# Kernel optimization log

Hardware: AMD Instinct MI355X
Metric: run time of the kernel (lower is better)

## Reference

```python
import jax, jax.numpy as jnp
import numpy as np

ORDER = 2  # diffusion steps per support
NUM_LAYERS = 2


def gconv(z, supports, W, b):
    # z: [B,N,C]; supports: [S,N,N]; concat [z, S1 z, S1^2 z, S2 z, S2^2 z] -> dense proj
    feats = [z]
    for si in range(supports.shape[0]):
        s = supports[si]
        zk = z
        for _ in range(ORDER):
            zk = jnp.einsum('mn,bnc->bmc', s, zk)
            feats.append(zk)
    zcat = jnp.concatenate(feats, axis=-1)  # [B,N,C*(1+S*ORDER)]
    return zcat @ W + b


def dcgru_cell(x, h, supports, Wg, bg, Wc, bc):
    H = h.shape[-1]
    zr = jax.nn.sigmoid(gconv(jnp.concatenate([x, h], axis=-1), supports, Wg, bg))
    z, r = zr[..., :H], zr[..., H:]
    hc = jnp.tanh(gconv(jnp.concatenate([x, r * h], axis=-1), supports, Wc, bc))
    return z * h + (1.0 - z) * hc


def setup_inputs() -> dict:
    key = jax.random.key(0)
    ks = jax.random.split(key, 32)
    B, T, N, D_IN, H = 64, 12, 325, 2, 128
    K = 1 + 2 * ORDER  # 5 diffusion matrices
    inp = {}
    inp['source'] = jax.random.normal(ks[0], (B, T, N, D_IN), jnp.float32)
    inp['targets'] = jax.random.normal(ks[1], (B, T, N, D_IN), jnp.float32)
    u = jax.random.uniform(ks[2], (2, N, N), jnp.float32)
    inp['supports'] = u / jnp.sum(u, axis=-1, keepdims=True)  # row-stochastic random walks
    sc = 0.05
    inp['enc_Wg0'] = sc * jax.random.normal(ks[3], ((D_IN + H) * K, 2 * H), jnp.float32)
    inp['enc_bg0'] = jnp.zeros((2 * H,), jnp.float32)
    inp['enc_Wc0'] = sc * jax.random.normal(ks[4], ((D_IN + H) * K, H), jnp.float32)
    inp['enc_bc0'] = jnp.zeros((H,), jnp.float32)
    inp['enc_Wg1'] = sc * jax.random.normal(ks[5], ((H + H) * K, 2 * H), jnp.float32)
    inp['enc_bg1'] = jnp.zeros((2 * H,), jnp.float32)
    inp['enc_Wc1'] = sc * jax.random.normal(ks[6], ((H + H) * K, H), jnp.float32)
    inp['enc_bc1'] = jnp.zeros((H,), jnp.float32)
    inp['dec_Wg0'] = sc * jax.random.normal(ks[7], ((D_IN + H) * K, 2 * H), jnp.float32)
    inp['dec_bg0'] = jnp.zeros((2 * H,), jnp.float32)
    inp['dec_Wc0'] = sc * jax.random.normal(ks[8], ((D_IN + H) * K, H), jnp.float32)
    inp['dec_bc0'] = jnp.zeros((H,), jnp.float32)
    inp['dec_Wg1'] = sc * jax.random.normal(ks[9], ((H + H) * K, 2 * H), jnp.float32)
    inp['dec_bg1'] = jnp.zeros((2 * H,), jnp.float32)
    inp['dec_Wc1'] = sc * jax.random.normal(ks[10], ((H + H) * K, H), jnp.float32)
    inp['dec_bc1'] = jnp.zeros((H,), jnp.float32)
    inp['Wp'] = sc * jax.random.normal(ks[11], (H, D_IN), jnp.float32)
    inp['bp'] = jnp.zeros((D_IN,), jnp.float32)
    return inp


def _forward(source, targets, supports,
             enc_Wg0, enc_bg0, enc_Wc0, enc_bc0, enc_Wg1, enc_bg1, enc_Wc1, enc_bc1,
             dec_Wg0, dec_bg0, dec_Wc0, dec_bc0, dec_Wg1, dec_bg1, dec_Wc1, dec_bc1,
             Wp, bp):
    B, T_in, N, D_in = source.shape
    T_out = targets.shape[1]
    enc_params = [(enc_Wg0, enc_bg0, enc_Wc0, enc_bc0), (enc_Wg1, enc_bg1, enc_Wc1, enc_bc1)]
    dec_params = [(dec_Wg0, dec_bg0, dec_Wc0, dec_bc0), (dec_Wg1, dec_bg1, dec_Wc1, dec_bc1)]

    # ---- encoder: per layer, scan over time ----
    cur = jnp.swapaxes(source, 0, 1)  # [T,B,N,C]
    enc_finals = []
    for (Wg, bg, Wc, bc) in enc_params:
        H = Wc.shape[-1]
        h0 = jnp.zeros((B, N, H), source.dtype)
        def step(h, xt, Wg=Wg, bg=bg, Wc=Wc, bc=bc):
            h2 = dcgru_cell(xt, h, supports, Wg, bg, Wc, bc)
            return h2, h2
        hT, hs = jax.lax.scan(step, h0, cur)
        enc_finals.append(hT)
        cur = hs

    # ---- decoder (teacher_forcing_ratio = 0 for determinism) ----
    out_dim = Wp.shape[-1]
    go = jnp.zeros((B, N, out_dim), source.dtype)  # GO symbol

    def dec_step(carry, _):
        states, cur_in = carry
        new_states = []
        x = cur_in
        for i, (Wg, bg, Wc, bc) in enumerate(dec_params):
            s = dcgru_cell(x, states[i], supports, Wg, bg, Wc, bc)
            x = s
            new_states.append(s)
        out = jnp.einsum('bnh,ho->bno', x, Wp) + bp  # [B,N,out_dim]
        return (tuple(new_states), out), out

    _, outs = jax.lax.scan(dec_step, (tuple(enc_finals), go), None, length=T_out)
    return jnp.swapaxes(outs, 0, 1)  # [B,T_out,N,out_dim]


def reference(source, targets, supports,
              enc_Wg0, enc_bg0, enc_Wc0, enc_bc0, enc_Wg1, enc_bg1, enc_Wc1, enc_bc1,
              dec_Wg0, dec_bg0, dec_Wc0, dec_bc0, dec_Wg1, dec_bg1, dec_Wc1, dec_bc1,
              Wp, bp):
    return _forward(source, targets, supports,
                    enc_Wg0, enc_bg0, enc_Wc0, enc_bc0, enc_Wg1, enc_bg1, enc_Wc1, enc_bc1,
                    dec_Wg0, dec_bg0, dec_Wc0, dec_bc0, dec_Wg1, dec_bg1, dec_Wc1, dec_bc1,
                    Wp, bp)
```

## Files before the change

kernel.cpp:

```cpp
#include <hip/hip_runtime.h>
#include <hip/hip_bf16.h>

#define B_  64
#define T_  12
#define N_  325
#define DIN 2
#define H_  128
#define BN  (B_*N_)
#define DPITCH 384
#define AROWS 384

typedef __hip_bfloat16 bf16;
typedef unsigned short u16;
typedef __attribute__((ext_vector_type(8))) short short8;
typedef __attribute__((ext_vector_type(4))) float f32x4;

__device__ __forceinline__ float b2f(bf16 v){ return __bfloat162float(v); }
__device__ __forceinline__ u16 f2b(float f){
    __hip_bfloat16 h = __float2bfloat16(f);
    return *reinterpret_cast<u16*>(&h);
}
__device__ __forceinline__ float ldf(const void* p, size_t i, int bf){
    return bf ? b2f(((const bf16*)p)[i]) : ((const float*)p)[i];
}

__device__ __forceinline__ void gl_lds16(const u16* g, u16* l){
    __builtin_amdgcn_global_load_lds(
        (const __attribute__((address_space(1))) unsigned int*)g,
        (__attribute__((address_space(3))) unsigned int*)l, 16, 0, 0);
}

struct FillCfg { u16 *F, *Ft; const float *x, *h; long xbs; int C, KCP, Cpad, Din, b0, nb; };
struct DiffCfg { u16* F; const u16* Ft; int C, KCP, Cpad, coff0, tpb, T, fcmax, nb; };
struct GemmCfg { const u16* Fb; const u16* Wt; const float* bias; float* zr; float* hb;
                 int KCP, rows, gy, ct, nb; };
struct RhCfg  { u16 *F, *Ft; const float *zr, *h; int KCP, Cpad, Din, b0, nb; };

__global__ void sniff(const void* __restrict__ sup, int* __restrict__ flag){
    if (threadIdx.x == 0 && blockIdx.x == 0){
        float sb = 0.f, sf = 0.f;
        for (int n = 0; n < N_; ++n){
            sb += b2f(((const bf16*)sup)[n]);
            sf += ((const float*)sup)[n];
        }
        float db = fabsf(sb - 1.f), df = fabsf(sf - 1.f);
        *flag = (db < df) ? 1 : 0;
    }
}

struct CvtArgs { const void* src[12]; float* dst[12]; int n[12]; };

__global__ void cvt_all(CvtArgs a, const int* __restrict__ flag){
    int ii = blockIdx.y;
    int i  = blockIdx.x*256 + threadIdx.x;
    if (i >= a.n[ii]) return;
    a.dst[ii][i] = ldf(a.src[ii], i, *flag);
}

__global__ void support_prep(const void* __restrict__ sup, const int* __restrict__ flag,
                             float* __restrict__ msq){
    int bf = *flag;
    int s = blockIdx.z;
    int m = blockIdx.y*16 + threadIdx.y;
    int n = blockIdx.x*16 + threadIdx.x;
    __shared__ float As[16][17], Bs[16][17];
    size_t base = (size_t)s*N_*N_;
    float acc = 0.f;
    for (int j0 = 0; j0 < N_; j0 += 16){
        As[threadIdx.y][threadIdx.x] = (m < N_ && j0+threadIdx.x < N_) ? ldf(sup, base + (size_t)m*N_ + j0+threadIdx.x, bf) : 0.f;
        Bs[threadIdx.y][threadIdx.x] = (j0+threadIdx.y < N_ && n < N_) ? ldf(sup, base + (size_t)(j0+threadIdx.y)*N_ + n, bf) : 0.f;
        __syncthreads();
        #pragma unroll
        for (int jj=0; jj<16; ++jj) acc += As[threadIdx.y][jj]*Bs[jj][threadIdx.x];
        __syncthreads();
    }
    if (m < N_ && n < N_){
        msq[(size_t)(2*s  )*N_*N_ + m*N_ + n] = ldf(sup, base + (size_t)m*N_ + n, bf);
        msq[(size_t)(2*s+1)*N_*N_ + m*N_ + n] = acc;
    }
}

__global__ void asq_prep(const float* __restrict__ msq, u16* __restrict__ asq){
    int idx = blockIdx.x*256 + threadIdx.x;
    int total = 4*AROWS*DPITCH;
    if (idx >= total) return;
    int col = idx % DPITCH;
    int rm  = idx / DPITCH;
    int m   = rm % AROWS;
    int k   = rm / AROWS;
    asq[idx] = (m < N_ && col < N_) ? f2b(msq[((size_t)k*N_ + m)*N_ + col]) : 0;
}

__global__ __launch_bounds__(256) void wtrans(const void* __restrict__ W, u16* __restrict__ Wt,
                                              int KC, int Nout, int KCpad,
                                              const int* __restrict__ flag){
    int bf = *flag;
    int k0 = blockIdx.x*64, c0 = blockIdx.y*64;
    int tid = threadIdx.x;
    __shared__ u16 T[64][72];
    #pragma unroll
    for (int it=0; it<2; ++it){
        int lin = it*256 + tid;
        int kl = lin >> 3, seg = lin & 7;
        int gk = k0 + kl, gc = c0 + seg*8;
        u16 tmp[8];
        #pragma unroll
        for (int e=0;e<8;++e) tmp[e] = (gk < KC) ? f2b(ldf(W, (size_t)gk*Nout + gc + e, bf)) : 0;
        *(uint4*)&T[kl][seg*8] = *(const uint4*)tmp;
    }
    __syncthreads();
    #pragma unroll
    for (int it=0; it<2; ++it){
        int lin = it*256 + tid;
        int cl = lin >> 3, seg = lin & 7;
        u16 tmp[8];
        #pragma unroll
        for (int j=0;j<8;++j) tmp[j] = T[seg*8+j][cl];
        *(uint4*)(Wt + (size_t)(c0+cl)*KCpad + k0 + seg*8) = *(const uint4*)tmp;
    }
}

__global__ __launch_bounds__(256) void fill_k(FillCfg ca, FillCfg cb, int na){
    int bi = blockIdx.x;
    FillCfg c = ca;
    if (bi >= na){ c = cb; bi -= na; }
    int gyc  = (c.C + 63) >> 6;
    int nblk = bi % 6;
    int rest = bi / 6;
    int cblk = rest % gyc;
    int bl   = rest / gyc;
    int bg = c.b0 + bl;
    int n0 = nblk*64, c0 = cblk*64;
    int tid = threadIdx.x;
    __shared__ u16 T[64][72];
    #pragma unroll
    for (int it=0; it<2; ++it){
        int lin = it*256 + tid;
        int nl = lin >> 3, seg = lin & 7;
        int gn = n0 + nl;
        u16 tmp[8];
        #pragma unroll
        for (int e=0;e<8;++e){
            int cc = c0 + seg*8 + e;
            float v = 0.f;
            if (gn < N_ && cc < c.C)
                v = (cc < c.Din) ? c.x[(size_t)bg*c.xbs + (size_t)gn*c.Din + cc]
                                 : c.h[((size_t)bg*N_ + gn)*H_ + (cc - c.Din)];
            tmp[e] = f2b(v);
        }
        *(uint4*)&T[nl][seg*8] = *(const uint4*)tmp;
        if (gn < N_){
            int cbase = c0 + seg*8;
            u16* dst = c.F + ((size_t)bl*N_ + gn)*c.KCP + cbase;
            if (cbase + 7 < c.C){
                *(uint4*)dst = *(const uint4*)tmp;
            } else {
                #pragma unroll
                for (int e=0;e<8;++e) if (cbase + e < c.C) dst[e] = tmp[e];
            }
        }
    }
    __syncthreads();
    #pragma unroll
    for (int it=0; it<2; ++it){
        int lin = it*256 + tid;
        int cl = lin >> 3, seg = lin & 7;
        if (c0 + cl < c.C){
            u16 tmp[8];
            #pragma unroll
            for (int j=0;j<8;++j) tmp[j] = T[seg*8+j][cl];
            *(uint4*)(c.Ft + ((size_t)bl*c.Cpad + (size_t)(c0+cl))*DPITCH + n0 + seg*8)
                = *(const uint4*)tmp;
        }
    }
}

__global__ __launch_bounds__(256) void rhfill_k(RhCfg ca, RhCfg cb, int na){
    int bi = blockIdx.x;
    RhCfg c = ca;
    if (bi >= na){ c = cb; bi -= na; }
    int nblk = bi % 6;
    int rest = bi / 6;
    int cblk = rest & 1;
    int bl   = rest >> 1;
    int bg = c.b0 + bl;
    int n0 = nblk*64, ch0 = cblk*64;
    int tid = threadIdx.x;
    __shared__ u16 T[64][72];
    #pragma unroll
    for (int it=0; it<2; ++it){
        int lin = it*256 + tid;
        int nl = lin >> 3, seg = lin & 7;
        int gn = n0 + nl;
        u16 tmp[8];
        if (gn < N_){
            size_t rloc = (size_t)bl*N_ + gn;
            size_t rg   = (size_t)bg*N_ + gn;
            const float* zp = c.zr + rloc*256 + 128 + ch0 + seg*8;
            const float* hp = c.h  + rg*128 + ch0 + seg*8;
            float4 z0 = *(const float4*)zp, z1 = *(const float4*)(zp+4);
            float4 h0 = *(const float4*)hp, h1 = *(const float4*)(hp+4);
            tmp[0]=f2b(z0.x*h0.x); tmp[1]=f2b(z0.y*h0.y);
            tmp[2]=f2b(z0.z*h0.z); tmp[3]=f2b(z0.w*h0.w);
            tmp[4]=f2b(z1.x*h1.x); tmp[5]=f2b(z1.y*h1.y);
            tmp[6]=f2b(z1.z*h1.z); tmp[7]=f2b(z1.w*h1.w);
            u16* fp = c.F + rloc*c.KCP + c.Din + ch0 + seg*8;
            #pragma unroll
            for (int e=0;e<4;++e){
                unsigned w = (unsigned)tmp[2*e] | ((unsigned)tmp[2*e+1] << 16);
                *(unsigned*)(fp + 2*e) = w;
            }
        } else {
            #pragma unroll
            for (int e=0;e<8;++e) tmp[e] = 0;
        }
        *(uint4*)&T[nl][seg*8] = *(const uint4*)tmp;
    }
    __syncthreads();
    #pragma unroll
    for (int it=0; it<2; ++it){
        int lin = it*256 + tid;
        int cl = lin >> 3, seg = lin & 7;
        u16 tmp[8];
        #pragma unroll
        for (int j=0;j<8;++j) tmp[j] = T[seg*8+j][cl];
        size_t row = (size_t)bl*c.Cpad + c.Din + ch0 + cl;
        *(uint4*)(c.Ft + row*DPITCH + n0 + seg*8) = *(const uint4*)tmp;
    }
}

__global__ __launch_bounds__(256) void diffuse_k(DiffCfg ca, DiffCfg cb, int na,
                                                 const u16* __restrict__ asq){
    int bi = blockIdx.x;
    DiffCfg c = ca;
    if (bi >= na){ c = cb; bi -= na; }
    int xcd = bi & 7, m8 = bi >> 3;
    int tg = m8 / 12, s = m8 % 12;
    int t = tg*8 + xcd;
    if (t >= c.T) return;
    int y = s % 3, k = s / 3;
    int fc0;
    if (c.tpb){
        int blb = t / c.tpb, tb = t - blb*c.tpb;
        fc0 = blb*c.Cpad + c.coff0 + tb*64;
    } else {
        fc0 = t*64;
    }
    int bl0  = fc0 / c.Cpad;
    int rem0 = fc0 - bl0*c.Cpad;

    const u16* A    = asq + (size_t)k*AROWS*DPITCH;
    const u16* Bt_g = c.Ft + (size_t)fc0*DPITCH;

    int m0 = y * 128;
    int tid = threadIdx.x;
    int wv = tid >> 6, lane = tid & 63, l15 = lane & 15, quad = lane >> 4;
    int lr = lane >> 3, ls = lane & 7;

    __shared__ u16 As[128*64];
    __shared__ u16 Bs[64*64];

    f32x4 acc[2][4];
    #pragma unroll
    for (int i2=0;i2<2;++i2)
        #pragma unroll
        for (int j=0;j<4;++j) acc[i2][j] = (f32x4){0.f,0.f,0.f,0.f};

    for (int k0 = 0; k0 < N_; k0 += 64){
        #pragma unroll
        for (int j=0;j<4;++j){
            int row = wv*32 + j*8 + lr;
            int seg = ls ^ lr;
            gl_lds16(A + (size_t)(m0+row)*DPITCH + k0 + seg*8, &As[(wv*32 + j*8)*64]);
        }
        #pragma unroll
        for (int j=0;j<2;++j){
            int row = wv*16 + j*8 + lr;
            int seg = ls ^ lr;
            gl_lds16(Bt_g + (size_t)row*DPITCH + k0 + seg*8, &Bs[(wv*16 + j*8)*64]);
        }
        __syncthreads();
        #pragma unroll
        for (int ks = 0; ks < 64; ks += 32){
            int sw = (((ks>>3) + quad) ^ (l15 & 7)) << 3;
            short8 a0 = *(const short8*)&As[(wv*32      + l15)*64 + sw];
            short8 a1 = *(const short8*)&As[(wv*32 + 16 + l15)*64 + sw];
            short8 b0 = *(const short8*)&Bs[(     l15)*64 + sw];
            short8 b1 = *(const short8*)&Bs[(16 + l15)*64 + sw];
            short8 b2 = *(const short8*)&Bs[(32 + l15)*64 + sw];
            short8 b3 = *(const short8*)&Bs[(48 + l15)*64 + sw];
            acc[0][0] = __builtin_amdgcn_mfma_f32_16x16x32_bf16(a0,b0,acc[0][0],0,0,0);
            acc[0][1] = __builtin_amdgcn_mfma_f32_16x16x32_bf16(a0,b1,acc[0][1],0,0,0);
            acc[0][2] = __builtin_amdgcn_mfma_f32_16x16x32_bf16(a0,b2,acc[0][2],0,0,0);
            acc[0][3] = __builtin_amdgcn_mfma_f32_16x16x32_bf16(a0,b3,acc[0][3],0,0,0);
            acc[1][0] = __builtin_amdgcn_mfma_f32_16x16x32_bf16(a1,b0,acc[1][0],0,0,0);
            acc[1][1] = __builtin_amdgcn_mfma_f32_16x16x32_bf16(a1,b1,acc[1][1],0,0,0);
            acc[1][2] = __builtin_amdgcn_mfma_f32_16x16x32_bf16(a1,b2,acc[1][2],0,0,0);
            acc[1][3] = __builtin_amdgcn_mfma_f32_16x16x32_bf16(a1,b3,acc[1][3],0,0,0);
        }
        __syncthreads();
    }
    #pragma unroll
    for (int j=0;j<4;++j){
        int d  = j*16 + l15;
        int cr = rem0 + d;
        int wrap = (cr >= c.Cpad) ? 1 : 0;
        int bl = bl0 + wrap;
        int cc = wrap ? (cr - c.Cpad) : cr;
        int ok = (fc0 + d) < c.fcmax;
        u16* Cm = c.F + (size_t)bl*N_*c.KCP + (size_t)(k+1)*c.C + cc;
        #pragma unroll
        for (int i2=0;i2<2;++i2){
            #pragma unroll
            for (int r=0;r<4;++r){
                int m = m0 + wv*32 + i2*16 + quad*4 + r;
                if (ok && m < N_) Cm[(size_t)m*c.KCP] = f2b(acc[i2][j][r]);
            }
        }
    }
}

template<int MODE>
__global__ __launch_bounds__(256) void gemm_k(GemmCfg ca, GemmCfg cb, int na){
    int bi = blockIdx.x;
    GemmCfg c = ca;
    if (bi >= na){ c = cb; bi -= na; }
    int xcd = bi & 7, q = bi >> 3;
    int cbk = q % c.ct;
    int rt  = (q / c.ct)*8 + xcd;
    if (rt >= c.gy) return;
    int r0 = rt * 128;
    int c0 = cbk * 64;
    int tid = threadIdx.x;
    int wv = tid >> 6, lane = tid & 63, l15 = lane & 15, quad = lane >> 4;
    int lr = lane >> 3, ls = lane & 7;

    __shared__ u16 As[128*64];
    __shared__ u16 Bs[64*64];

    f32x4 acc[2][4];
    #pragma unroll
    for (int i2=0;i2<2;++i2)
        #pragma unroll
        for (int j=0;j<4;++j) acc[i2][j] = (f32x4){0.f,0.f,0.f,0.f};

    for (int k0 = 0; k0 < c.KCP; k0 += 64){
        #pragma unroll
        for (int j=0;j<4;++j){
            int row = wv*32 + j*8 + lr;
            int seg = ls ^ lr;
            gl_lds16(c.Fb + (size_t)(r0+row)*c.KCP + k0 + seg*8, &As[(wv*32 + j*8)*64]);
        }
        #pragma unroll
        for (int j=0;j<2;++j){
            int row = wv*16 + j*8 + lr;
            int seg = ls ^ lr;
            gl_lds16(c.Wt + (size_t)(c0+row)*c.KCP + k0 + seg*8, &Bs[(wv*16 + j*8)*64]);
        }
        __syncthreads();
        #pragma unroll
        for (int ks = 0; ks < 64; ks += 32){
            int sw = (((ks>>3) + quad) ^ (l15 & 7)) << 3;
            short8 a0 = *(const short8*)&As[(wv*32      + l15)*64 + sw];
            short8 a1 = *(const short8*)&As[(wv*32 + 16 + l15)*64 + sw];
            short8 b0 = *(const short8*)&Bs[(     l15)*64 + sw];
            short8 b1 = *(const short8*)&Bs[(16 + l15)*64 + sw];
            short8 b2 = *(const short8*)&Bs[(32 + l15)*64 + sw];
            short8 b3 = *(const short8*)&Bs[(48 + l15)*64 + sw];
            acc[0][0] = __builtin_amdgcn_mfma_f32_16x16x32_bf16(a0,b0,acc[0][0],0,0,0);
            acc[0][1] = __builtin_amdgcn_mfma_f32_16x16x32_bf16(a0,b1,acc[0][1],0,0,0);
            acc[0][2] = __builtin_amdgcn_mfma_f32_16x16x32_bf16(a0,b2,acc[0][2],0,0,0);
            acc[0][3] = __builtin_amdgcn_mfma_f32_16x16x32_bf16(a0,b3,acc[0][3],0,0,0);
            acc[1][0] = __builtin_amdgcn_mfma_f32_16x16x32_bf16(a1,b0,acc[1][0],0,0,0);
            acc[1][1] = __builtin_amdgcn_mfma_f32_16x16x32_bf16(a1,b1,acc[1][1],0,0,0);
            acc[1][2] = __builtin_amdgcn_mfma_f32_16x16x32_bf16(a1,b2,acc[1][2],0,0,0);
            acc[1][3] = __builtin_amdgcn_mfma_f32_16x16x32_bf16(a1,b3,acc[1][3],0,0,0);
        }
        __syncthreads();
    }
    #pragma unroll
    for (int i2=0;i2<2;++i2){
        #pragma unroll
        for (int j=0;j<4;++j){
            int cc = c0 + j*16 + l15;
            #pragma unroll
            for (int r=0;r<4;++r){
                int gr = r0 + wv*32 + i2*16 + quad*4 + r;
                if (gr >= c.rows) continue;
                float v = acc[i2][j][r] + c.bias[cc];
                if (MODE == 0){
                    v = 1.f/(1.f + __expf(-v));
                    c.zr[(size_t)gr*256 + cc] = v;
                } else {
                    float hc   = tanhf(v);
                    float z    = c.zr[(size_t)gr*256 + cc];
                    float hold = c.hb[(size_t)gr*128 + cc];
                    c.hb[(size_t)gr*128 + cc] = z*hold + (1.f - z)*hc;
                }
            }
        }
    }
}

__global__ __launch_bounds__(256) void proj(const float* __restrict__ h1,
                                            const float* __restrict__ Wp,
                                            const float* __restrict__ bp,
                                            float* __restrict__ xdec,
                                            float* __restrict__ out, int t){
    int row  = blockIdx.x * 4 + (threadIdx.x >> 6);
    int lane = threadIdx.x & 63;
    float v0 = h1[(size_t)row*128 + lane];
    float v1 = h1[(size_t)row*128 + 64 + lane];
    float w00 = Wp[lane*2+0],      w01 = Wp[lane*2+1];
    float w10 = Wp[(64+lane)*2+0], w11 = Wp[(64+lane)*2+1];
    float a0 = v0*w00 + v1*w10;
    float a1 = v0*w01 + v1*w11;
    #pragma unroll
    for (int off=32; off>0; off>>=1){
        a0 += __shfl_down(a0, off);
        a1 += __shfl_down(a1, off);
    }
    if (lane == 0){
        a0 += bp[0];
        a1 += bp[1];
        xdec[(size_t)row*2+0] = a0;
        xdec[(size_t)row*2+1] = a1;
        int b = row / N_, n = row % N_;
        size_t o = ((size_t)(b*T_ + t)*N_ + n)*2;
        out[o]   = a0;
        out[o+1] = a1;
    }
}

struct Layer {
    u16 *F, *Ft; float *zr; float *h;
    const u16 *Wg, *Wc; const float *bg, *bc;
    int C, KCP, Din, Cpad;
};

extern "C" void kernel_launch(void* const* d_in, const int* in_sizes, int n_in,
                              void* d_out, int out_size, void* d_ws, size_t ws_size,
                              hipStream_t stream){
    float* out = (float*)d_out;

    char* pb = (char*)d_ws;
    auto alloc = [&](size_t bytes)->void*{
        void* r = (void*)pb;
        pb += (bytes + 255) & ~(size_t)255;
        return r;
    };

    int* flag = (int*)alloc(16);
    sniff<<<1, 64, 0, stream>>>(d_in[2], flag);

    const int idxs[11] = {0,4,6,8,10,12,14,16,18,19,20};
    float* cw[21] = {nullptr};
    CvtArgs ca;
    int maxn = 0;
    for (int ii = 0; ii < 11; ++ii){
        int i = idxs[ii];
        int n = in_sizes[i];
        cw[i] = (float*)alloc((size_t)n*4);
        ca.src[ii] = d_in[i];
        ca.dst[ii] = cw[i];
        ca.n[ii]   = n;
        if (n > maxn) maxn = n;
    }
    cvt_all<<<dim3((maxn+255)/256, 11), 256, 0, stream>>>(ca, flag);
    const float* src = cw[0];

    float* msq  = (float*)alloc((size_t)4*N_*N_*4);
    float* h0   = (float*)alloc((size_t)BN*H_*4);
    float* h1   = (float*)alloc((size_t)BN*H_*4);
    float* xdec = (float*)alloc((size_t)BN*DIN*4);
    u16*   asq  = (u16*)alloc((size_t)4*AROWS*DPITCH*2);

    const int widx[8]  = {3,5,7,9,11,13,15,17};
    const int wKC[8]   = {650,650,1280,1280,650,650,1280,1280};
    const int wNout[8] = {256,128,256,128,256,128,256,128};
    u16* wt[8];
    for (int i=0;i<8;++i){
        int KCpad = (wKC[i] + 63) & ~63;
        wt[i] = (u16*)alloc((size_t)wNout[i]*KCpad*2);
        wtrans<<<dim3(KCpad/64, wNout[i]/64), 256, 0, stream>>>(d_in[widx[i]], wt[i], wKC[i], wNout[i], KCpad, flag);
    }

    {
        dim3 g((N_+15)/16, (N_+15)/16, 2), b(16,16);
        support_prep<<<g, b, 0, stream>>>(d_in[2], flag, msq);
        int tot = 4*AROWS*DPITCH;
        asq_prep<<<dim3((tot+255)/256), 256, 0, stream>>>(msq, asq);
    }
    hipMemsetAsync(h0, 0, sizeof(float)*(size_t)BN*H_*2, stream);

    size_t fixed = (size_t)(pb - (char*)d_ws);
    size_t need0 = (size_t)BN*256*4 + (size_t)BN*704*2  + (size_t)B_*130*DPITCH*2;
    size_t need1 = (size_t)BN*256*4 + (size_t)BN*1280*2 + (size_t)B_*256*DPITCH*2;
    bool dual = (fixed + need0 + need1 + (4<<20)) <= ws_size;

    auto mkFill = [&](Layer& L, const float* x, long xbs, int b0, int Bc)->FillCfg{
        return FillCfg{L.F, L.Ft, x, L.h, xbs, L.C, L.KCP, L.Cpad, L.Din, b0,
                       6*((L.C+63)>>6)*Bc};
    };
    auto mkD1 = [&](Layer& L, int Bc)->DiffCfg{
        int fcmax = Bc*L.Cpad;
        int T = fcmax >> 6;
        return DiffCfg{L.F, L.Ft, L.C, L.KCP, L.Cpad, 0, 0, T, fcmax,
                       12*(((T+7)/8)*8)};
    };
    auto mkD2 = [&](Layer& L, int Bc)->DiffCfg{
        int T = Bc*2;
        return DiffCfg{L.F, L.Ft, L.C, L.KCP, L.Cpad, L.Din, 2, T, Bc*L.Cpad,
                       12*(((T+7)/8)*8)};
    };
    auto mkG0 = [&](Layer& L, int b0, int Bc)->GemmCfg{
        int rows = Bc*N_, gy = (rows+127)/128;
        return GemmCfg{L.F, L.Wg, L.bg, L.zr, L.h + (size_t)b0*N_*H_,
                       L.KCP, rows, gy, 4, 8*((gy+7)/8)*4};
    };
    auto mkG1 = [&](Layer& L, int b0, int Bc)->GemmCfg{
        int rows = Bc*N_, gy = (rows+127)/128;
        return GemmCfg{L.F, L.Wc, L.bc, L.zr, L.h + (size_t)b0*N_*H_,
                       L.KCP, rows, gy, 2, 8*((gy+7)/8)*2};
    };
    auto mkRh = [&](Layer& L, int b0, int Bc)->RhCfg{
        return RhCfg{L.F, L.Ft, L.zr, L.h, L.KCP, L.Cpad, L.Din, b0, 12*Bc};
    };
    auto runCellSeq = [&](Layer& L, const float* x, long xbs, int b0, int Bc){
        FillCfg f = mkFill(L, x, xbs, b0, Bc);
        fill_k<<<dim3(f.nb), 256, 0, stream>>>(f, f, f.nb);
        DiffCfg d1 = mkD1(L, Bc);
        diffuse_k<<<dim3(d1.nb), 256, 0, stream>>>(d1, d1, d1.nb, asq);
        GemmCfg g0 = mkG0(L, b0, Bc);
        gemm_k<0><<<dim3(g0.nb), 256, 0, stream>>>(g0, g0, g0.nb);
        RhCfg r = mkRh(L, b0, Bc);
        rhfill_k<<<dim3(r.nb), 256, 0, stream>>>(r, r, r.nb);
        DiffCfg d2 = mkD2(L, Bc);
        diffuse_k<<<dim3(d2.nb), 256, 0, stream>>>(d2, d2, d2.nb, asq);
        GemmCfg g1 = mkG1(L, b0, Bc);
        gemm_k<1><<<dim3(g1.nb), 256, 0, stream>>>(g1, g1, g1.nb);
    };

    if (dual){
        float* zr0 = (float*)alloc((size_t)BN*256*4);
        u16*   F0  = (u16*)alloc((size_t)BN*704*2);
        u16*   Ft0 = (u16*)alloc((size_t)B_*130*DPITCH*2);
        float* zr1 = (float*)alloc((size_t)BN*256*4);
        u16*   F1  = (u16*)alloc((size_t)BN*1280*2);
        u16*   Ft1 = (u16*)alloc((size_t)B_*256*DPITCH*2);
        alloc(1<<19);

        hipMemsetAsync(F0, 0, (size_t)BN*704*2, stream);

        Layer E0{F0, Ft0, zr0, h0, wt[0], wt[1], cw[4],  cw[6],  130, 704,  2,   130};
        Layer E1{F1, Ft1, zr1, h1, wt[2], wt[3], cw[8],  cw[10], 256, 1280, 128, 256};
        Layer D0{F0, Ft0, zr0, h0, wt[4], wt[5], cw[12], cw[14], 130, 704,  2,   130};
        Layer D1{F1, Ft1, zr1, h1, wt[6], wt[7], cw[16], cw[18], 256, 1280, 128, 256};

        for (int s = 0; s <= T_; ++s){
            bool has0 = (s < T_), has1 = (s >= 1);
            const float* x0 = src + (size_t)s*N_*DIN;
            FillCfg f0 = mkFill(E0, x0, (long)T_*N_*DIN, 0, B_);
            FillCfg f1 = mkFill(E1, h0, (long)N_*H_,     0, B_);
            if (has0 && has1) fill_k<<<dim3(f0.nb+f1.nb),256,0,stream>>>(f0, f1, f0.nb);
            else if (has0)    fill_k<<<dim3(f0.nb),256,0,stream>>>(f0, f0, f0.nb);
            else              fill_k<<<dim3(f1.nb),256,0,stream>>>(f1, f1, f1.nb);

            DiffCfg a1 = mkD1(E0, B_), b1 = mkD1(E1, B_);
            if (has0 && has1) diffuse_k<<<dim3(a1.nb+b1.nb),256,0,stream>>>(a1, b1, a1.nb, asq);
            else if (has0)    diffuse_k<<<dim3(a1.nb),256,0,stream>>>(a1, a1, a1.nb, asq);
            else              diffuse_k<<<dim3(b1.nb),256,0,stream>>>(b1, b1, b1.nb, asq);

            GemmCfg ga = mkG0(E0, 0, B_), gb = mkG0(E1, 0, B_);
            if (has0 && has1) gemm_k<0><<<dim3(ga.nb+gb.nb),256,0,stream>>>(ga, gb, ga.nb);
            else if (has0)    gemm_k<0><<<dim3(ga.nb),256,0,stream>>>(ga, ga, ga.nb);
            else              gemm_k<0><<<dim3(gb.nb),256,0,stream>>>(gb, gb, gb.nb);

            RhCfg ra = mkRh(E0, 0, B_), rb = mkRh(E1, 0, B_);
            if (has0 && has1) rhfill_k<<<dim3(ra.nb+rb.nb),256,0,stream>>>(ra, rb, ra.nb);
            else if (has0)    rhfill_k<<<dim3(ra.nb),256,0,stream>>>(ra, ra, ra.nb);
            else              rhfill_k<<<dim3(rb.nb),256,0,stream>>>(rb, rb, rb.nb);

            DiffCfg a2 = mkD2(E0, B_), b2 = mkD2(E1, B_);
            if (has0 && has1) diffuse_k<<<dim3(a2.nb+b2.nb),256,0,stream>>>(a2, b2, a2.nb, asq);
            else if (has0)    diffuse_k<<<dim3(a2.nb),256,0,stream>>>(a2, a2, a2.nb, asq);
            else              diffuse_k<<<dim3(b2.nb),256,0,stream>>>(b2, b2, b2.nb, asq);

            GemmCfg ha = mkG1(E0, 0, B_), hb = mkG1(E1, 0, B_);
            if (has0 && has1) gemm_k<1><<<dim3(ha.nb+hb.nb),256,0,stream>>>(ha, hb, ha.nb);
            else if (has0)    gemm_k<1><<<dim3(ha.nb),256,0,stream>>>(ha, ha, ha.nb);
            else              gemm_k<1><<<dim3(hb.nb),256,0,stream>>>(hb, hb, hb.nb);
        }

        hipMemsetAsync(xdec, 0, sizeof(float)*(size_t)BN*DIN, stream);
        for (int t = 0; t < T_; ++t){
            runCellSeq(D0, xdec, (long)N_*DIN, 0, B_);
            runCellSeq(D1, h0,   (long)N_*H_,  0, B_);
            proj<<<dim3(BN/4), 256, 0, stream>>>(h1, cw[19], cw[20], xdec, out, t);
        }
    } else {
        size_t perb = (size_t)N_*1280*2 + (size_t)N_*256*4 + (size_t)256*DPITCH*2;
        int Bc = 64;
        while (Bc > 2 && fixed + (1<<20) + (size_t)Bc*perb > ws_size) Bc >>= 1;
        float* zr = (float*)alloc((size_t)Bc*N_*256*4);
        u16*   F  = (u16*)alloc((size_t)Bc*N_*1280*2);
        u16*   Ft = (u16*)alloc((size_t)Bc*256*DPITCH*2);
        alloc(1<<19);

        hipMemsetAsync(F, 0, (size_t)Bc*N_*1280*2, stream);

        Layer SE0{F, Ft, zr, h0, wt[0], wt[1], cw[4],  cw[6],  130, 704,  2,   130};
        Layer SE1{F, Ft, zr, h1, wt[2], wt[3], cw[8],  cw[10], 256, 1280, 128, 256};
        Layer SD0{F, Ft, zr, h0, wt[4], wt[5], cw[12], cw[14], 130, 704,  2,   130};
        Layer SD1{F, Ft, zr, h1, wt[6], wt[7], cw[16], cw[18], 256, 1280, 128, 256};

        for (int t = 0; t < T_; ++t){
            for (int b0 = 0; b0 < B_; b0 += Bc)
                runCellSeq(SE0, src + (size_t)t*N_*DIN, (long)T_*N_*DIN, b0, Bc);
            for (int b0 = 0; b0 < B_; b0 += Bc)
                runCellSeq(SE1, h0, (long)N_*H_, b0, Bc);
        }
        hipMemsetAsync(xdec, 0, sizeof(float)*(size_t)BN*DIN, stream);
        for (int t = 0; t < T_; ++t){
            for (int b0 = 0; b0 < B_; b0 += Bc)
                runCellSeq(SD0, xdec, (long)N_*DIN, b0, Bc);
            for (int b0 = 0; b0 < B_; b0 += Bc)
                runCellSeq(SD1, h0, (long)N_*H_, b0, Bc);
            proj<<<dim3(BN/4), 256, 0, stream>>>(h1, cw[19], cw[20], xdec, out, t);
        }
    }
}
```

Measured before the change: 5.319 ms.

## Fuse reset-gate r*h fill into gate GEMM epilogue with double-buffered features

Removes the separate rhfill kernel. The gate GEMM's epilogue now computes r*h for the reset half and writes it directly into a second feature buffer and its transposed copy through shared memory. The fill and diffusion kernels duplicate the x-dependent columns into that second buffer, and zr storage shrinks to z only. This saves one launch per cell and a round trip of the reset gate through global memory, at the cost of twice the feature-buffer memory and extra duplicate stores.

New measurement: 5.604 ms. 5.3% more time.

```diff
diff --git a/kernel.cpp b/kernel.cpp
--- a/kernel.cpp
+++ b/kernel.cpp
@@ -30,11 +30,10 @@
         (__attribute__((address_space(3))) unsigned int*)l, 16, 0, 0);
 }
 
-struct FillCfg { u16 *F, *Ft; const float *x, *h; long xbs; int C, KCP, Cpad, Din, b0, nb; };
-struct DiffCfg { u16* F; const u16* Ft; int C, KCP, Cpad, coff0, tpb, T, fcmax, nb; };
+struct FillCfg { u16 *F, *F2, *Ft; const float *x, *h; long xbs; int C, KCP, Cpad, Din, b0, nb; };
+struct DiffCfg { u16 *F, *Fd; const u16* Ft; int C, KCP, Cpad, coff0, tpb, T, fcmax, Din, nb; };
 struct GemmCfg { const u16* Fb; const u16* Wt; const float* bias; float* zr; float* hb;
-                 int KCP, rows, gy, ct, nb; };
-struct RhCfg  { u16 *F, *Ft; const float *zr, *h; int KCP, Cpad, Din, b0, nb; };
+                 u16 *Fw, *Ft; int KCP, rows, gy, ct, Din, Cpad, nb; };
 
 __global__ void sniff(const void* __restrict__ sup, int* __restrict__ flag){
     if (threadIdx.x == 0 && blockIdx.x == 0){
@@ -151,12 +150,22 @@
         *(uint4*)&T[nl][seg*8] = *(const uint4*)tmp;
         if (gn < N_){
             int cbase = c0 + seg*8;
-            u16* dst = c.F + ((size_t)bl*N_ + gn)*c.KCP + cbase;
+            size_t roff = ((size_t)bl*N_ + gn)*c.KCP + cbase;
+            u16* dst = c.F + roff;
             if (cbase + 7 < c.C){
                 *(uint4*)dst = *(const uint4*)tmp;
             } else {
                 #pragma unroll
                 for (int e=0;e<8;++e) if (cbase + e < c.C) dst[e] = tmp[e];
+            }
+            if (cbase < c.Din){
+                u16* dst2 = c.F2 + roff;
+                if (cbase + 7 < c.Din){
+                    *(uint4*)dst2 = *(const uint4*)tmp;
+                } else {
+                    #pragma unroll
+                    for (int e=0;e<8;++e) if (cbase + e < c.Din) dst2[e] = tmp[e];
+                }
             }
         }
     }
@@ -172,60 +181,6 @@
             *(uint4*)(c.Ft + ((size_t)bl*c.Cpad + (size_t)(c0+cl))*DPITCH + n0 + seg*8)
                 = *(const uint4*)tmp;
         }
-    }
-}
-
-__global__ __launch_bounds__(256) void rhfill_k(RhCfg ca, RhCfg cb, int na){
-    int bi = blockIdx.x;
-    RhCfg c = ca;
-    if (bi >= na){ c = cb; bi -= na; }
-    int nblk = bi % 6;
-    int rest = bi / 6;
-    int cblk = rest & 1;
-    int bl   = rest >> 1;
-    int bg = c.b0 + bl;
-    int n0 = nblk*64, ch0 = cblk*64;
-    int tid = threadIdx.x;
-    __shared__ u16 T[64][72];
-    #pragma unroll
-    for (int it=0; it<2; ++it){
-        int lin = it*256 + tid;
-        int nl = lin >> 3, seg = lin & 7;
-        int gn = n0 + nl;
-        u16 tmp[8];
-        if (gn < N_){
-            size_t rloc = (size_t)bl*N_ + gn;
-            size_t rg   = (size_t)bg*N_ + gn;
-            const float* zp = c.zr + rloc*256 + 128 + ch0 + seg*8;
-            const float* hp = c.h  + rg*128 + ch0 + seg*8;
-            float4 z0 = *(const float4*)zp, z1 = *(const float4*)(zp+4);
-            float4 h0 = *(const float4*)hp, h1 = *(const float4*)(hp+4);
-            tmp[0]=f2b(z0.x*h0.x); tmp[1]=f2b(z0.y*h0.y);
-            tmp[2]=f2b(z0.z*h0.z); tmp[3]=f2b(z0.w*h0.w);
-            tmp[4]=f2b(z1.x*h1.x); tmp[5]=f2b(z1.y*h1.y);
-            tmp[6]=f2b(z1.z*h1.z); tmp[7]=f2b(z1.w*h1.w);
-            u16* fp = c.F + rloc*c.KCP + c.Din + ch0 + seg*8;
-            #pragma unroll
-            for (int e=0;e<4;++e){
-                unsigned w = (unsigned)tmp[2*e] | ((unsigned)tmp[2*e+1] << 16);
-                *(unsigned*)(fp + 2*e) = w;
-            }
-        } else {
-            #pragma unroll
-            for (int e=0;e<8;++e) tmp[e] = 0;
-        }
-        *(uint4*)&T[nl][seg*8] = *(const uint4*)tmp;
-    }
-    __syncthreads();
-    #pragma unroll
-    for (int it=0; it<2; ++it){
-        int lin = it*256 + tid;
-        int cl = lin >> 3, seg = lin & 7;
-        u16 tmp[8];
-        #pragma unroll
-        for (int j=0;j<8;++j) tmp[j] = T[seg*8+j][cl];
-        size_t row = (size_t)bl*c.Cpad + c.Din + ch0 + cl;
-        *(uint4*)(c.Ft + row*DPITCH + n0 + seg*8) = *(const uint4*)tmp;
     }
 }
 
@@ -308,13 +263,20 @@
         int bl = bl0 + wrap;
         int cc = wrap ? (cr - c.Cpad) : cr;
         int ok = (fc0 + d) < c.fcmax;
-        u16* Cm = c.F + (size_t)bl*N_*c.KCP + (size_t)(k+1)*c.C + cc;
+        size_t off = (size_t)bl*N_*c.KCP + (size_t)(k+1)*c.C + cc;
+        u16* Cm = c.F  + off;
+        u16* Cd = c.Fd + off;
+        int dup = cc < c.Din;
         #pragma unroll
         for (int i2=0;i2<2;++i2){
             #pragma unroll
             for (int r=0;r<4;++r){
                 int m = m0 + wv*32 + i2*16 + quad*4 + r;
-                if (ok && m < N_) Cm[(size_t)m*c.KCP] = f2b(acc[i2][j][r]);
+                if (ok && m < N_){
+                    u16 v = f2b(acc[i2][j][r]);
+                    Cm[(size_t)m*c.KCP] = v;
+                    if (dup) Cd[(size_t)m*c.KCP] = v;
+                }
             }
         }
     }
@@ -335,8 +297,9 @@
     int wv = tid >> 6, lane = tid & 63, l15 = lane & 15, quad = lane >> 4;
     int lr = lane >> 3, ls = lane & 7;
 
-    __shared__ u16 As[128*64];
-    __shared__ u16 Bs[64*64];
+    __shared__ u16 SM[128*64 + 64*64];
+    u16* As = SM;
+    u16* Bs = SM + 128*64;
 
     f32x4 acc[2][4];
     #pragma unroll
@@ -378,24 +341,96 @@
         }
         __syncthreads();
     }
-    #pragma unroll
-    for (int i2=0;i2<2;++i2){
-        #pragma unroll
-        for (int j=0;j<4;++j){
-            int cc = c0 + j*16 + l15;
+
+    if (MODE == 1){
+        #pragma unroll
+        for (int i2=0;i2<2;++i2){
             #pragma unroll
-            for (int r=0;r<4;++r){
-                int gr = r0 + wv*32 + i2*16 + quad*4 + r;
-                if (gr >= c.rows) continue;
-                float v = acc[i2][j][r] + c.bias[cc];
-                if (MODE == 0){
-                    v = 1.f/(1.f + __expf(-v));
-                    c.zr[(size_t)gr*256 + cc] = v;
-                } else {
+            for (int j=0;j<4;++j){
+                int cc = c0 + j*16 + l15;
+                #pragma unroll
+                for (int r=0;r<4;++r){
+                    int gr = r0 + wv*32 + i2*16 + quad*4 + r;
+                    if (gr >= c.rows) continue;
+                    float v = acc[i2][j][r] + c.bias[cc];
                     float hc   = tanhf(v);
-                    float z    = c.zr[(size_t)gr*256 + cc];
+                    float z    = c.zr[(size_t)gr*128 + cc];
                     float hold = c.hb[(size_t)gr*128 + cc];
                     c.hb[(size_t)gr*128 + cc] = z*hold + (1.f - z)*hc;
+                }
+            }
+        }
+    } else if (c0 < 128){
+        #pragma unroll
+        for (int i2=0;i2<2;++i2){
+            #pragma unroll
+            for (int j=0;j<4;++j){
+                int cc = c0 + j*16 + l15;
+                #pragma unroll
+                for (int r=0;r<4;++r){
+                    int gr = r0 + wv*32 + i2*16 + quad*4 + r;
+                    if (gr >= c.rows) continue;
+                    float v = acc[i2][j][r] + c.bias[cc];
+                    c.zr[(size_t)gr*128 + cc] = 1.f/(1.f + __expf(-v));
+                }
+            }
+        }
+    } else {
+        int ch0 = c0 - 128;
+        #pragma unroll
+        for (int j=0;j<4;++j){
+            int chl = j*16 + l15;
+            int ch  = ch0 + chl;
+            float bs = c.bias[c0 + chl];
+            #pragma unroll
+            for (int i2=0;i2<2;++i2){
+                #pragma unroll
+                for (int r=0;r<4;++r){
+                    int grl = wv*32 + i2*16 + quad*4 + r;
+                    int gr  = r0 + grl;
+                    u16 pb = 0;
+                    if (gr < c.rows){
+                        float v  = acc[i2][j][r] + bs;
+                        float rr = 1.f/(1.f + __expf(-v));
+                        float hv = c.hb[(size_t)gr*128 + ch];
+                        pb = f2b(rr * hv);
+                        c.Fw[(size_t)gr*c.KCP + c.Din + ch] = pb;
+                    }
+                    SM[chl*136 + grl] = pb;
+                }
+            }
+        }
+        __syncthreads();
+        int cl = tid >> 2, part = tid & 3;
+        int ch = ch0 + cl;
+        #pragma unroll
+        for (int c4=0;c4<4;++c4){
+            int grl = part*32 + c4*8;
+            int gr  = r0 + grl;
+            if (gr >= c.rows) continue;
+            int bl = gr / N_;
+            int n  = gr - bl*N_;
+            u16* frow = c.Ft + ((size_t)bl*c.Cpad + c.Din + ch)*DPITCH;
+            const u16* src = &SM[cl*136 + grl];
+            if (gr + 7 < c.rows && n + 8 <= N_){
+                if ((n & 7) == 0){
+                    *(uint4*)(frow + n) = *(const uint4*)src;
+                } else if ((n & 1) == 0){
+                    #pragma unroll
+                    for (int e=0;e<4;++e)
+                        *(unsigned*)(frow + n + 2*e) = *(const unsigned*)(src + 2*e);
+                } else {
+                    #pragma unroll
+                    for (int e=0;e<8;++e) frow[n + e] = src[e];
+                }
+            } else {
+                for (int e=0;e<8;++e){
+                    int g = gr + e;
+                    if (g < c.rows){
+                        int b2 = g / N_;
+                        int n2 = g - b2*N_;
+                        c.Ft[((size_t)b2*c.Cpad + c.Din + ch)*DPITCH + n2] = src[e];
+                    }
                 }
             }
         }
@@ -433,7 +468,7 @@
 }
 
 struct Layer {
-    u16 *F, *Ft; float *zr; float *h;
+    u16 *F, *F2, *Ft; float *zr; float *h;
     const u16 *Wg, *Wc; const float *bg, *bc;
     int C, KCP, Din, Cpad;
 };
@@ -494,37 +529,36 @@
     hipMemsetAsync(h0, 0, sizeof(float)*(size_t)BN*H_*2, stream);
 
     size_t fixed = (size_t)(pb - (char*)d_ws);
-    size_t need0 = (size_t)BN*256*4 + (size_t)BN*704*2  + (size_t)B_*130*DPITCH*2;
-    size_t need1 = (size_t)BN*256*4 + (size_t)BN*1280*2 + (size_t)B_*256*DPITCH*2;
+    size_t need0 = (size_t)BN*128*4 + 2*(size_t)BN*704*2  + (size_t)B_*130*DPITCH*2;
+    size_t need1 = (size_t)BN*128*4 + 2*(size_t)BN*1280*2 + (size_t)B_*256*DPITCH*2;
     bool dual = (fixed + need0 + need1 + (4<<20)) <= ws_size;
 
     auto mkFill = [&](Layer& L, const float* x, long xbs, int b0, int Bc)->FillCfg{
-        return FillCfg{L.F, L.Ft, x, L.h, xbs, L.C, L.KCP, L.Cpad, L.Din, b0,
+        return FillCfg{L.F, L.F2, L.Ft, x, L.h, xbs, L.C, L.KCP, L.Cpad, L.Din, b0,
                        6*((L.C+63)>>6)*Bc};
     };
     auto mkD1 = [&](Layer& L, int Bc)->DiffCfg{
         int fcmax = Bc*L.Cpad;
         int T = fcmax >> 6;
-        return DiffCfg{L.F, L.Ft, L.C, L.KCP, L.Cpad, 0, 0, T, fcmax,
+        return DiffCfg{L.F, L.F2, L.Ft, L.C, L.KCP, L.Cpad, 0, 0, T, fcmax, L.Din,
                        12*(((T+7)/8)*8)};
     };
     auto mkD2 = [&](Layer& L, int Bc)->DiffCfg{
         int T = Bc*2;
-        return DiffCfg{L.F, L.Ft, L.C, L.KCP, L.Cpad, L.Din, 2, T, Bc*L.Cpad,
+        return DiffCfg{L.F2, L.F2, L.Ft, L.C, L.KCP, L.Cpad, L.Din, 2, T, Bc*L.Cpad, 0,
                        12*(((T+7)/8)*8)};
     };
     auto mkG0 = [&](Layer& L, int b0, int Bc)->GemmCfg{
         int rows = Bc*N_, gy = (rows+127)/128;
         return GemmCfg{L.F, L.Wg, L.bg, L.zr, L.h + (size_t)b0*N_*H_,
-                       L.KCP, rows, gy, 4, 8*((gy+7)/8)*4};
+                       L.F2, L.Ft, L.KCP, rows, gy, 4, L.Din, L.Cpad,
+                       8*((gy+7)/8)*4};
     };
     auto mkG1 = [&](Layer& L, int b0, int Bc)->GemmCfg{
         int rows = Bc*N_, gy = (rows+127)/128;
-        return GemmCfg{L.F, L.Wc, L.bc, L.zr, L.h + (size_t)b0*N_*H_,
-                       L.KCP, rows, gy, 2, 8*((gy+7)/8)*2};
-    };
-    auto mkRh = [&](Layer& L, int b0, int Bc)->RhCfg{
-        return RhCfg{L.F, L.Ft, L.zr, L.h, L.KCP, L.Cpad, L.Din, b0, 12*Bc};
+        return GemmCfg{L.F2, L.Wc, L.bc, L.zr, L.h + (size_t)b0*N_*H_,
+                       L.F2, L.Ft, L.KCP, rows, gy, 2, L.Din, L.Cpad,
+                       8*((gy+7)/8)*2};
     };
     auto runCellSeq = [&](Layer& L, const float* x, long xbs, int b0, int Bc){
         FillCfg f = mkFill(L, x, xbs, b0, Bc);
@@ -533,8 +567,6 @@
         diffuse_k<<<dim3(d1.nb), 256, 0, stream>>>(d1, d1, d1.nb, asq);
         GemmCfg g0 = mkG0(L, b0, Bc);
         gemm_k<0><<<dim3(g0.nb), 256, 0, stream>>>(g0, g0, g0.nb);
-        RhCfg r = mkRh(L, b0, Bc);
-        rhfill_k<<<dim3(r.nb), 256, 0, stream>>>(r, r, r.nb);
         DiffCfg d2 = mkD2(L, Bc);
         diffuse_k<<<dim3(d2.nb), 256, 0, stream>>>(d2, d2, d2.nb, asq);
         GemmCfg g1 = mkG1(L, b0, Bc);
@@ -542,20 +574,23 @@
     };
 
     if (dual){
-        float* zr0 = (float*)alloc((size_t)BN*256*4);
-        u16*   F0  = (u16*)alloc((size_t)BN*704*2);
+        float* zr0 = (float*)alloc((size_t)BN*128*4);
+        u16*   F0a = (u16*)alloc((size_t)BN*704*2);
+        u16*   F0b = (u16*)alloc((size_t)BN*704*2);
         u16*   Ft0 = (u16*)alloc((size_t)B_*130*DPITCH*2);
-        float* zr1 = (float*)alloc((size_t)BN*256*4);
-        u16*   F1  = (u16*)alloc((size_t)BN*1280*2);
+        float* zr1 = (float*)alloc((size_t)BN*128*4);
+        u16*   F1a = (u16*)alloc((size_t)BN*1280*2);
+        u16*   F1b = (u16*)alloc((size_t)BN*1280*2);
         u16*   Ft1 = (u16*)alloc((size_t)B_*256*DPITCH*2);
         alloc(1<<19);
 
-        hipMemsetAsync(F0, 0, (size_t)BN*704*2, stream);
-
-        Layer E0{F0, Ft0, zr0, h0, wt[0], wt[1], cw[4],  cw[6],  130, 704,  2,   130};
-        Layer E1{F1, Ft1, zr1, h1, wt[2], wt[3], cw[8],  cw[10], 256, 1280, 128, 256};
-        Layer D0{F0, Ft0, zr0, h0, wt[4], wt[5], cw[12], cw[14], 130, 704,  2,   130};
-        Layer D1{F1, Ft1, zr1, h1, wt[6], wt[7], cw[16], cw[18], 256, 1280, 128, 256};
+        hipMemsetAsync(F0a, 0, (size_t)BN*704*2, stream);
+        hipMemsetAsync(F0b, 0, (size_t)BN*704*2, stream);
+
+        Layer E0{F0a, F0b, Ft0, zr0, h0, wt[0], wt[1], cw[4],  cw[6],  130, 704,  2,   130};
+        Layer E1{F1a, F1b, Ft1, zr1, h1, wt[2], wt[3], cw[8],  cw[10], 256, 1280, 128, 256};
+        Layer D0{F0a, F0b, Ft0, zr0, h0, wt[4], wt[5], cw[12], cw[14], 130, 704,  2,   130};
+        Layer D1{F1a, F1b, Ft1, zr1, h1, wt[6], wt[7], cw[16], cw[18], 256, 1280, 128, 256};
 
         for (int s = 0; s <= T_; ++s){
             bool has0 = (s < T_), has1 = (s >= 1);
@@ -576,11 +611,6 @@
             else if (has0)    gemm_k<0><<<dim3(ga.nb),256,0,stream>>>(ga, ga, ga.nb);
             else              gemm_k<0><<<dim3(gb.nb),256,0,stream>>>(gb, gb, gb.nb);
 
-            RhCfg ra = mkRh(E0, 0, B_), rb = mkRh(E1, 0, B_);
-            if (has0 && has1) rhfill_k<<<dim3(ra.nb+rb.nb),256,0,stream>>>(ra, rb, ra.nb);
-            else if (has0)    rhfill_k<<<dim3(ra.nb),256,0,stream>>>(ra, ra, ra.nb);
-            else              rhfill_k<<<dim3(rb.nb),256,0,stream>>>(rb, rb, rb.nb);
-
             DiffCfg a2 = mkD2(E0, B_), b2 = mkD2(E1, B_);
             if (has0 && has1) diffuse_k<<<dim3(a2.nb+b2.nb),256,0,stream>>>(a2, b2, a2.nb, asq);
             else if (has0)    diffuse_k<<<dim3(a2.nb),256,0,stream>>>(a2, a2, a2.nb, asq);
@@ -599,20 +629,22 @@
             proj<<<dim3(BN/4), 256, 0, stream>>>(h1, cw[19], cw[20], xdec, out, t);
         }
     } else {
-        size_t perb = (size_t)N_*1280*2 + (size_t)N_*256*4 + (size_t)256*DPITCH*2;
+        size_t perb = (size_t)N_*(2*1280*2 + 128*4) + (size_t)256*DPITCH*2;
         int Bc = 64;
         while (Bc > 2 && fixed + (1<<20) + (size_t)Bc*perb > ws_size) Bc >>= 1;
-        float* zr = (float*)alloc((size_t)Bc*N_*256*4);
-        u16*   F  = (u16*)alloc((size_t)Bc*N_*1280*2);
+        float* zr = (float*)alloc((size_t)Bc*N_*128*4);
+        u16*   Fa = (u16*)alloc((size_t)Bc*N_*1280*2);
+        u16*   Fb = (u16*)alloc((size_t)Bc*N_*1280*2);
         u16*   Ft = (u16*)alloc((size_t)Bc*256*DPITCH*2);
         alloc(1<<19);
 
-        hipMemsetAsync(F, 0, (size_t)Bc*N_*1280*2, stream);
-
-        Layer SE0{F, Ft, zr, h0, wt[0], wt[1], cw[4],  cw[6],  130, 704,  2,   130};
-        Layer SE1{F, Ft, zr, h1, wt[2], wt[3], cw[8],  cw[10], 256, 1280, 128, 256};
-        Layer SD0{F, Ft, zr, h0, wt[4], wt[5], cw[12], cw[14], 130, 704,  2,   130};
-        Layer SD1{F, Ft, zr, h1, wt[6], wt[7], cw[16], cw[18], 256, 1280, 128, 256};
+        hipMemsetAsync(Fa, 0, (size_t)Bc*N_*1280*2, stream);
+        hipMemsetAsync(Fb, 0, (size_t)Bc*N_*1280*2, stream);
+
+        Layer SE0{Fa, Fb, Ft, zr, h0, wt[0], wt[1], cw[4],  cw[6],  130, 704,  2,   130};
+        Layer SE1{Fa, Fb, Ft, zr, h1, wt[2], wt[3], cw[8],  cw[10], 256, 1280, 128, 256};
+        Layer SD0{Fa, Fb, Ft, zr, h0, wt[4], wt[5], cw[12], cw[14], 130, 704,  2,   130};
+        Layer SD1{Fa, Fb, Ft, zr, h1, wt[6], wt[7], cw[16], cw[18], 256, 1280, 128, 256};
 
         for (int t = 0; t < T_; ++t){
             for (int b0 = 0; b0 < B_; b0 += Bc)
```
